# Performance work log

Measured on AMD Instinct MI355X. Metric: run time of the kernel, lower is better.

## Reference

```python
import jax, jax.numpy as jnp
import numpy as np

B, L, NS, D, M = 64, 200, 1000, 128, 50


def setup_inputs() -> dict:
    key = jax.random.key(0)
    ks = jax.random.split(key, 12)
    s = np.sqrt(2.0 / D).astype(np.float32)  # kaiming_normal scale for Mk/Mv0
    lw = np.sqrt(1.0 / D).astype(np.float32)
    return {
        "skills": jax.random.randint(ks[0], (B, L), 0, NS),
        "responses": jax.random.randint(ks[1], (B, L), 0, 2),
        "k_emb": jax.random.normal(ks[2], (NS, D), jnp.float32) * 0.02,
        "v_emb": jax.random.normal(ks[3], (2 * NS, D), jnp.float32) * 0.02,
        "Mk": jax.random.normal(ks[4], (M, D), jnp.float32) * s,
        "Mv0": jax.random.normal(ks[5], (M, D), jnp.float32) * s,
        "e_W": jax.random.normal(ks[6], (D, D), jnp.float32) * lw,
        "e_b": jnp.zeros((D,), jnp.float32),
        "a_W": jax.random.normal(ks[7], (D, D), jnp.float32) * lw,
        "a_b": jnp.zeros((D,), jnp.float32),
        "f_W": jax.random.normal(ks[8], (D, 2 * D), jnp.float32) * np.sqrt(1.0 / (2 * D)).astype(np.float32),
        "f_b": jnp.zeros((D,), jnp.float32),
        "p_W": jax.random.normal(ks[9], (1, D), jnp.float32) * lw,
        "p_b": jnp.zeros((1,), jnp.float32),
    }


def _dkvmn_forward(skills, responses, k_emb, v_emb, Mk, Mv0,
                   e_W, e_b, a_W, a_b, f_W, f_b, p_W, p_b):
    masked_r = responses * (responses > -1).astype(responses.dtype)
    x = skills + NS * masked_r                      # [B,L] combined (skill,response) id
    k = k_emb[skills]                               # [B,L,D]
    v = v_emb[x]                                    # [B,L,D]
    w = jax.nn.softmax(jnp.einsum('bld,md->blm', k, Mk), axis=-1)  # [B,L,M]
    e = jax.nn.sigmoid(v @ e_W.T + e_b)             # erase  [B,L,D]
    a = jnp.tanh(v @ a_W.T + a_b)                   # add    [B,L,D]

    def step(Mvt, wea):
        wt, et, at = wea                            # [B,M], [B,D], [B,D]
        u = wt[:, :, None]                          # [B,M,1]
        new = Mvt * (1.0 - u * et[:, None, :]) + u * at[:, None, :]
        return new, Mvt                             # emit PRE-update state (Mv[:, :-1])

    Mv_init = jnp.broadcast_to(Mv0[None], (B, M, D))
    _, Mv_pre = jax.lax.scan(
        step, Mv_init,
        (w.transpose(1, 0, 2), e.transpose(1, 0, 2), a.transpose(1, 0, 2)))
    # Mv_pre: [L,B,M,D]; weighted read of pre-update memory
    read = jnp.einsum('blm,lbmd->bld', w, Mv_pre)   # [B,L,D]
    f = jnp.tanh(jnp.concatenate([read, k], axis=-1) @ f_W.T + f_b)  # [B,L,D]
    p = jax.nn.sigmoid(f @ p_W.T + p_b)[..., 0]     # [B,L] (dropout off: eval)
    return p[:, 1:]                                 # pred, [B,L-1]


def reference(skills, responses, k_emb, v_emb, Mk, Mv0,
              e_W, e_b, a_W, a_b, f_W, f_b, p_W, p_b):
    return _dkvmn_forward(skills, responses, k_emb, v_emb, Mk, Mv0,
                          e_W, e_b, a_W, a_b, f_W, f_b, p_W, p_b)
```

## Files before the change

### kernel.cpp

```cpp
#include <hip/hip_runtime.h>
#include <hip/hip_bf16.h>

#define Bb 64
#define Ll 200
#define NSs 1000
#define Dd 128
#define Mm 50

__device__ __forceinline__ float bcast_lane(float v, int l) {
    return __int_as_float(__builtin_amdgcn_readlane(__float_as_int(v), l));
}

__global__ void __launch_bounds__(256) kern_wea(
        const int* __restrict__ skills,
        const int* __restrict__ responses,
        const float* __restrict__ k_emb,
        const float* __restrict__ v_emb,
        const float* __restrict__ Mk,
        const float* __restrict__ e_W, const float* __restrict__ e_b,
        const float* __restrict__ a_W, const float* __restrict__ a_b,
        float* __restrict__ w_out,
        float* __restrict__ e_out, float* __restrict__ a_out) {
    __shared__ float smem[12672];
    int tid = threadIdx.x;

    if (blockIdx.x >= 400) {
        int blk = blockIdx.x - 400;
        float (*mk)[Dd + 4] = (float(*)[Dd + 4])smem;
        float (*kr)[Dd + 4] = (float(*)[Dd + 4])(smem + 6600);

        for (int lin = tid; lin < (Mm * Dd) / 4; lin += 256) {
            float4 f = ((const float4*)Mk)[lin];
            *(float4*)&mk[lin >> 5][(lin & 31) * 4] = f;
        }
        for (int lin = tid; lin < 16 * 32; lin += 256) {
            int r  = lin >> 5;
            int c4 = lin & 31;
            int bl = blk * 16 + r;
            float4 f = ((const float4*)(k_emb + (size_t)skills[bl] * Dd))[c4];
            *(float4*)&kr[r][c4 * 4] = f;
        }
        __syncthreads();

        int wave = tid >> 6, lane = tid & 63;
        int mmr  = (lane < Mm) ? lane : 0;
        float acc[4] = {0.f, 0.f, 0.f, 0.f};
#pragma unroll 2
        for (int q = 0; q < 32; ++q) {
            float4 mkv = *(const float4*)&mk[mmr][q * 4];
#pragma unroll
            for (int i = 0; i < 4; ++i) {
                float4 kv = *(const float4*)&kr[wave * 4 + i][q * 4];
                acc[i] = fmaf(mkv.x, kv.x, acc[i]);
                acc[i] = fmaf(mkv.y, kv.y, acc[i]);
                acc[i] = fmaf(mkv.z, kv.z, acc[i]);
                acc[i] = fmaf(mkv.w, kv.w, acc[i]);
            }
        }
#pragma unroll
        for (int i = 0; i < 4; ++i) {
            float logit = (lane < Mm) ? acc[i] : -1e30f;
            float mx = logit;
            for (int off = 32; off > 0; off >>= 1) mx = fmaxf(mx, __shfl_down(mx, off));
            mx = __shfl(mx, 0);
            float ex = (lane < Mm) ? expf(logit - mx) : 0.f;
            float sm = ex;
            for (int off = 32; off > 0; off >>= 1) sm += __shfl_down(sm, off);
            sm = __shfl(sm, 0);
            int bl = blk * 16 + wave * 4 + i;
            if (lane < Mm) w_out[(size_t)bl * Mm + lane] = ex / sm;
        }
        return;
    }

    int blk = blockIdx.x;
    float (*vt)[Dd + 4] = (float(*)[Dd + 4])smem;
    float (*wt)[Dd + 4] = (float(*)[Dd + 4])(smem + 4224);

#pragma unroll
    for (int i = 0; i < 4; ++i) {
        int lin = i * 256 + tid;
        int r   = lin >> 5;
        int c4  = lin & 31;
        int bl  = blk * 32 + r;
        int rr  = responses[bl];
        int x   = skills[bl] + NSs * ((rr > -1) ? rr : 0);
        float4 f = ((const float4*)(v_emb + (size_t)x * Dd))[c4];
        *(float4*)&vt[r][c4 * 4] = f;
    }
    __syncthreads();

    int wave = tid >> 6, lane = tid & 63;
    int pg = lane >> 3, og = lane & 7;

    for (int s = 0; s < 4; ++s) {
        int base_row = wave * 64 + s * 16;
        bool is_e    = base_row < 128;
        const float* W = is_e ? e_W : a_W;
        int wrow0 = is_e ? base_row : base_row - 128;

#pragma unroll
        for (int i = 0; i < 8; ++i) {
            int lin = i * 64 + lane;
            int r   = lin >> 5;
            int c4  = lin & 31;
            float4 f = ((const float4*)(W + (size_t)(wrow0 + r) * Dd))[c4];
            *(float4*)&wt[wave * 16 + r][c4 * 4] = f;
        }

        float acc[4][2] = {};
#pragma unroll 2
        for (int q = 0; q < 32; ++q) {
            float4 av[4], bv[2];
#pragma unroll
            for (int i = 0; i < 4; ++i) av[i] = *(const float4*)&vt[pg + 8 * i][q * 4];
#pragma unroll
            for (int j = 0; j < 2; ++j) bv[j] = *(const float4*)&wt[wave * 16 + og + 8 * j][q * 4];
#pragma unroll
            for (int i = 0; i < 4; ++i)
#pragma unroll
                for (int j = 0; j < 2; ++j) {
                    acc[i][j] = fmaf(av[i].x, bv[j].x, acc[i][j]);
                    acc[i][j] = fmaf(av[i].y, bv[j].y, acc[i][j]);
                    acc[i][j] = fmaf(av[i].z, bv[j].z, acc[i][j]);
                    acc[i][j] = fmaf(av[i].w, bv[j].w, acc[i][j]);
                }
        }

        float* dst = is_e ? e_out : a_out;
#pragma unroll
        for (int j = 0; j < 2; ++j) {
            int row = wrow0 + og + 8 * j;
            float bias = (is_e ? e_b : a_b)[row];
#pragma unroll
            for (int i = 0; i < 4; ++i) {
                int bl = blk * 32 + pg + 8 * i;
                float v = acc[i][j] + bias;
                dst[(size_t)bl * Dd + row] = is_e ? (1.f / (1.f + expf(-v))) : tanhf(v);
            }
        }
    }
}

#define PQ_LOAD(S, tt) do { int _t = (tt);                                   \
    if (_t < T) { size_t _bl = blBase + _t;                                  \
        w##S = (lane < Mm) ? w_ws[_bl * Mm + lane] : 0.f;                    \
        e##S = e_ws[_bl * Dd + d];  a##S = a_ws[_bl * Dd + d]; } } while (0)

#define PQ_BODY(S) do {                                                      \
    _Pragma("unroll")                                                        \
    for (int m = 0; m < Mm; ++m) {                                           \
        float wm = bcast_lane(w##S, m);                                      \
        float A  = fmaf(-wm, e##S, 1.f);                                     \
        Q[m] = fmaf(A, Q[m], wm * a##S);                                     \
        P[m] *= A; } } while (0)

__global__ void __launch_bounds__(128) kern_scan_pq(
        const float* __restrict__ w_ws,
        const float* __restrict__ e_ws,
        const float* __restrict__ a_ws,
        float* __restrict__ P_ws, float* __restrict__ Q_ws,
        int C, int T) {
    int b = blockIdx.x / C, c = blockIdx.x % C;
    int d = threadIdx.x;
    int lane = d & 63;
    float P[Mm], Q[Mm];
#pragma unroll
    for (int m = 0; m < Mm; ++m) { P[m] = 1.f; Q[m] = 0.f; }

    size_t blBase = (size_t)b * Ll + (size_t)c * T;
    float w0 = 0.f, e0 = 0.f, a0 = 0.f;
    float w1 = 0.f, e1 = 0.f, a1 = 0.f;
    float w2 = 0.f, e2 = 0.f, a2 = 0.f;
    PQ_LOAD(0, 0);
    PQ_LOAD(1, 1);
    for (int tt = 0; tt < T; tt += 3) {
        PQ_LOAD(2, tt + 2);  PQ_BODY(0);
        if (tt + 1 < T) { PQ_LOAD(0, tt + 3);  PQ_BODY(1); }
        if (tt + 2 < T) { PQ_LOAD(1, tt + 4);  PQ_BODY(2); }
    }
    size_t base = ((size_t)(b * C + c)) * (Mm * Dd) + d;
#pragma unroll
    for (int m = 0; m < Mm; ++m) {
        P_ws[base + m * Dd] = P[m];
        Q_ws[base + m * Dd] = Q[m];
    }
}

template <int CC>
__global__ void kern_scan_comb_t(
        const float* __restrict__ Mv0,
        const float* __restrict__ P_ws, const float* __restrict__ Q_ws,
        float* __restrict__ S_ws) {
    int idx = blockIdx.x * 256 + threadIdx.x;
    int b   = idx / (Mm * Dd);
    int md  = idx % (Mm * Dd);
    float Pr[CC - 1], Qr[CC - 1];
#pragma unroll
    for (int c = 0; c < CC - 1; ++c) {
        size_t pq = ((size_t)(b * CC + c)) * (Mm * Dd) + md;
        Pr[c] = P_ws[pq];
        Qr[c] = Q_ws[pq];
    }
    float s = Mv0[md];
#pragma unroll
    for (int c = 0; c < CC - 1; ++c) {
        s = fmaf(Pr[c], s, Qr[c]);
        S_ws[((size_t)(b * (CC - 1) + c)) * (Mm * Dd) + md] = s;
    }
}

#define RD_BODY(S, tt) do {                                                  \
    float acc0 = 0.f, acc1 = 0.f;                                            \
    _Pragma("unroll")                                                        \
    for (int m = 0; m < Mm; m += 2) {                                        \
        float wm0 = bcast_lane(w##S, m);                                     \
        float wm1 = bcast_lane(w##S, m + 1);                                 \
        acc0 = fmaf(wm0, mv[m], acc0);                                       \
        mv[m] = fmaf(wm0, fmaf(-e##S, mv[m], a##S), mv[m]);                  \
        acc1 = fmaf(wm1, mv[m + 1], acc1);                                   \
        mv[m + 1] = fmaf(wm1, fmaf(-e##S, mv[m + 1], a##S), mv[m + 1]);      \
    }                                                                        \
    read_ws[(blBase + (tt)) * Dd + d] = acc0 + acc1;                         \
    } while (0)

__global__ void __launch_bounds__(128) kern_scan_rd(
        const float* __restrict__ Mv0,
        const float* __restrict__ S_ws,
        const float* __restrict__ w_ws,
        const float* __restrict__ e_ws,
        const float* __restrict__ a_ws,
        float* __restrict__ read_ws,
        int C, int T) {
    int b = blockIdx.x / C, c = blockIdx.x % C;
    int d = threadIdx.x;
    int lane = d & 63;
    float mv[Mm];
    if (c == 0) {
#pragma unroll
        for (int m = 0; m < Mm; ++m) mv[m] = Mv0[m * Dd + d];
    } else {
        size_t sb = ((size_t)(b * (C - 1) + (c - 1))) * (Mm * Dd) + d;
#pragma unroll
        for (int m = 0; m < Mm; ++m) mv[m] = S_ws[sb + m * Dd];
    }

    size_t blBase = (size_t)b * Ll + (size_t)c * T;
    float w0 = 0.f, e0 = 0.f, a0 = 0.f;
    float w1 = 0.f, e1 = 0.f, a1 = 0.f;
    float w2 = 0.f, e2 = 0.f, a2 = 0.f;
    PQ_LOAD(0, 0);
    PQ_LOAD(1, 1);
    for (int tt = 0; tt < T; tt += 3) {
        PQ_LOAD(2, tt + 2);  RD_BODY(0, tt);
        if (tt + 1 < T) { PQ_LOAD(0, tt + 3);  RD_BODY(1, tt + 1); }
        if (tt + 2 < T) { PQ_LOAD(1, tt + 4);  RD_BODY(2, tt + 2); }
    }
}

__global__ void __launch_bounds__(256) kern_out(
        const int* __restrict__ skills,
        const float* __restrict__ read_ws,
        const float* __restrict__ k_emb,
        const float* __restrict__ f_W, const float* __restrict__ f_b,
        const float* __restrict__ p_W, const float* __restrict__ p_b,
        float* __restrict__ out) {
    __shared__ float ct[32][2 * Dd + 4];
    __shared__ float wt[4][16][Dd + 4];
    __shared__ float pf[32][8];
    int tid = threadIdx.x;
    int blk = blockIdx.x;

#pragma unroll
    for (int i = 0; i < 8; ++i) {
        int lin = i * 256 + tid;
        int r   = lin >> 6;
        int c4  = lin & 63;
        int idx = blk * 32 + r;
        int b   = idx / (Ll - 1);
        int l   = idx % (Ll - 1) + 1;
        int bl  = b * Ll + l;
        float4 f;
        if (c4 < 32) f = ((const float4*)(read_ws + (size_t)bl * Dd))[c4];
        else         f = ((const float4*)(k_emb + (size_t)skills[bl] * Dd))[c4 - 32];
        *(float4*)&ct[r][c4 * 4] = f;
    }
    ((float*)pf)[tid] = 0.f;
    __syncthreads();

    int wave = tid >> 6, lane = tid & 63;
    int pg = lane >> 3, og = lane & 7;

    float ppart[4] = {0.f, 0.f, 0.f, 0.f};
    for (int sub = 0; sub < 2; ++sub) {
        float acc[4][2] = {};
        for (int h = 0; h < 2; ++h) {
#pragma unroll
            for (int i = 0; i < 8; ++i) {
                int lin = i * 64 + lane;
                int r   = lin >> 5;
                int c4  = lin & 31;
                float4 f = ((const float4*)(f_W +
                            (size_t)(wave * 32 + sub * 16 + r) * (2 * Dd)))[h * 32 + c4];
                *(float4*)&wt[wave][r][c4 * 4] = f;
            }
#pragma unroll 2
            for (int q = 0; q < 32; ++q) {
                int k = h * 128 + q * 4;
                float4 av[4], bv[2];
#pragma unroll
                for (int i = 0; i < 4; ++i) av[i] = *(const float4*)&ct[pg + 8 * i][k];
#pragma unroll
                for (int j = 0; j < 2; ++j) bv[j] = *(const float4*)&wt[wave][og + 8 * j][q * 4];
#pragma unroll
                for (int i = 0; i < 4; ++i)
#pragma unroll
                    for (int j = 0; j < 2; ++j) {
                        acc[i][j] = fmaf(av[i].x, bv[j].x, acc[i][j]);
                        acc[i][j] = fmaf(av[i].y, bv[j].y, acc[i][j]);
                        acc[i][j] = fmaf(av[i].z, bv[j].z, acc[i][j]);
                        acc[i][j] = fmaf(av[i].w, bv[j].w, acc[i][j]);
                    }
            }
        }
#pragma unroll
        for (int j = 0; j < 2; ++j) {
            int row = wave * 32 + sub * 16 + og + 8 * j;
            float fb = f_b[row];
            float pw = p_W[row];
#pragma unroll
            for (int i = 0; i < 4; ++i)
                ppart[i] = fmaf(tanhf(acc[i][j] + fb), pw, ppart[i]);
        }
    }
#pragma unroll
    for (int i = 0; i < 4; ++i) {
        float v = ppart[i];
        for (int off = 4; off > 0; off >>= 1) v += __shfl_down(v, off, 8);
        if (og == 0) pf[pg + 8 * i][wave] = v;
    }
    __syncthreads();
    if (tid < 32) {
        float s = pf[tid][0] + pf[tid][1] + pf[tid][2] + pf[tid][3] + p_b[0];
        out[blk * 32 + tid] = 1.f / (1.f + expf(-s));
    }
}

extern "C" void kernel_launch(void* const* d_in, const int* in_sizes, int n_in,
                              void* d_out, int out_size, void* d_ws, size_t ws_size,
                              hipStream_t stream) {
    const int*   skills    = (const int*)  d_in[0];
    const int*   responses = (const int*)  d_in[1];
    const float* k_emb     = (const float*)d_in[2];
    const float* v_emb     = (const float*)d_in[3];
    const float* Mk        = (const float*)d_in[4];
    const float* Mv0       = (const float*)d_in[5];
    const float* e_W       = (const float*)d_in[6];
    const float* e_b       = (const float*)d_in[7];
    const float* a_W       = (const float*)d_in[8];
    const float* a_b       = (const float*)d_in[9];
    const float* f_W       = (const float*)d_in[10];
    const float* f_b       = (const float*)d_in[11];
    const float* p_W       = (const float*)d_in[12];
    const float* p_b       = (const float*)d_in[13];
    (void)in_sizes; (void)n_in; (void)out_size;

    float* out = (float*)d_out;

    float* ws      = (float*)d_ws;
    float* w_ws    = ws;
    float* e_ws    = w_ws + (size_t)Bb * Ll * Mm;
    float* a_ws    = e_ws + (size_t)Bb * Ll * Dd;
    float* read_ws = a_ws + (size_t)Bb * Ll * Dd;
    float* extra   = read_ws + (size_t)Bb * Ll * Dd;

    const size_t baseF = (size_t)Bb * Ll * Mm + 3 * (size_t)Bb * Ll * Dd;
    const size_t BMD   = (size_t)Bb * Mm * Dd;
    int C = 1;
    const int cands[3] = {8, 5, 2};
    for (int i = 0; i < 3; ++i) {
        size_t need = (baseF + BMD * (3 * (size_t)cands[i] - 1)) * sizeof(float);
        if (ws_size >= need) { C = cands[i]; break; }
    }
    int T = Ll / C;
    float* P_ws = extra;
    float* Q_ws = P_ws + BMD * C;
    float* S_ws = Q_ws + BMD * C;

    kern_wea<<<400 + Bb * Ll / 16, 256, 0, stream>>>(skills, responses, k_emb, v_emb, Mk,
                                                     e_W, e_b, a_W, a_b, w_ws, e_ws, a_ws);
    if (C > 1) {
        kern_scan_pq<<<Bb * C, 128, 0, stream>>>(w_ws, e_ws, a_ws, P_ws, Q_ws, C, T);
        int cgrid = (int)(BMD / 256);
        if      (C == 8) kern_scan_comb_t<8><<<cgrid, 256, 0, stream>>>(Mv0, P_ws, Q_ws, S_ws);
        else if (C == 5) kern_scan_comb_t<5><<<cgrid, 256, 0, stream>>>(Mv0, P_ws, Q_ws, S_ws);
        else             kern_scan_comb_t<2><<<cgrid, 256, 0, stream>>>(Mv0, P_ws, Q_ws, S_ws);
    }
    kern_scan_rd<<<Bb * C, 128, 0, stream>>>(Mv0, S_ws, w_ws, e_ws, a_ws, read_ws, C, T);
    kern_out<<<Bb * (Ll - 1) / 32, 256, 0, stream>>>(skills, read_ws, k_emb,
                                                     f_W, f_b, p_W, p_b, out);
}
```

Before: 184.4 us.

## Fuse all five stages into one persistent kernel with grid barriers

Replaces the five separate launches (projection, chunked scan P/Q, combine, scan-read, output) with one persistent kernel of 256 blocks. The stages are separated by atomic grid-wide barriers and each stage loops over its work items. The aim is to remove launch gaps and tail effects between the small kernels. In exchange it adds barrier spin costs, fixes the chunk count at 8 without checking workspace size, and relies on all 256 blocks being resident at once.

```diff
diff --git a/kernel.cpp b/kernel.cpp
--- a/kernel.cpp
+++ b/kernel.cpp
@@ -6,140 +6,30 @@
 #define NSs 1000
 #define Dd 128
 #define Mm 50
+#define CC 8
+#define TT 25
+#define NBLK 256
 
 __device__ __forceinline__ float bcast_lane(float v, int l) {
     return __int_as_float(__builtin_amdgcn_readlane(__float_as_int(v), l));
 }
 
-__global__ void __launch_bounds__(256) kern_wea(
-        const int* __restrict__ skills,
-        const int* __restrict__ responses,
-        const float* __restrict__ k_emb,
-        const float* __restrict__ v_emb,
-        const float* __restrict__ Mk,
-        const float* __restrict__ e_W, const float* __restrict__ e_b,
-        const float* __restrict__ a_W, const float* __restrict__ a_b,
-        float* __restrict__ w_out,
-        float* __restrict__ e_out, float* __restrict__ a_out) {
-    __shared__ float smem[12672];
-    int tid = threadIdx.x;
-
-    if (blockIdx.x >= 400) {
-        int blk = blockIdx.x - 400;
-        float (*mk)[Dd + 4] = (float(*)[Dd + 4])smem;
-        float (*kr)[Dd + 4] = (float(*)[Dd + 4])(smem + 6600);
-
-        for (int lin = tid; lin < (Mm * Dd) / 4; lin += 256) {
-            float4 f = ((const float4*)Mk)[lin];
-            *(float4*)&mk[lin >> 5][(lin & 31) * 4] = f;
-        }
-        for (int lin = tid; lin < 16 * 32; lin += 256) {
-            int r  = lin >> 5;
-            int c4 = lin & 31;
-            int bl = blk * 16 + r;
-            float4 f = ((const float4*)(k_emb + (size_t)skills[bl] * Dd))[c4];
-            *(float4*)&kr[r][c4 * 4] = f;
-        }
-        __syncthreads();
-
-        int wave = tid >> 6, lane = tid & 63;
-        int mmr  = (lane < Mm) ? lane : 0;
-        float acc[4] = {0.f, 0.f, 0.f, 0.f};
-#pragma unroll 2
-        for (int q = 0; q < 32; ++q) {
-            float4 mkv = *(const float4*)&mk[mmr][q * 4];
-#pragma unroll
-            for (int i = 0; i < 4; ++i) {
-                float4 kv = *(const float4*)&kr[wave * 4 + i][q * 4];
-                acc[i] = fmaf(mkv.x, kv.x, acc[i]);
-                acc[i] = fmaf(mkv.y, kv.y, acc[i]);
-                acc[i] = fmaf(mkv.z, kv.z, acc[i]);
-                acc[i] = fmaf(mkv.w, kv.w, acc[i]);
-            }
-        }
-#pragma unroll
-        for (int i = 0; i < 4; ++i) {
-            float logit = (lane < Mm) ? acc[i] : -1e30f;
-            float mx = logit;
-            for (int off = 32; off > 0; off >>= 1) mx = fmaxf(mx, __shfl_down(mx, off));
-            mx = __shfl(mx, 0);
-            float ex = (lane < Mm) ? expf(logit - mx) : 0.f;
-            float sm = ex;
-            for (int off = 32; off > 0; off >>= 1) sm += __shfl_down(sm, off);
-            sm = __shfl(sm, 0);
-            int bl = blk * 16 + wave * 4 + i;
-            if (lane < Mm) w_out[(size_t)bl * Mm + lane] = ex / sm;
-        }
-        return;
-    }
-
-    int blk = blockIdx.x;
-    float (*vt)[Dd + 4] = (float(*)[Dd + 4])smem;
-    float (*wt)[Dd + 4] = (float(*)[Dd + 4])(smem + 4224);
-
-#pragma unroll
-    for (int i = 0; i < 4; ++i) {
-        int lin = i * 256 + tid;
-        int r   = lin >> 5;
-        int c4  = lin & 31;
-        int bl  = blk * 32 + r;
-        int rr  = responses[bl];
-        int x   = skills[bl] + NSs * ((rr > -1) ? rr : 0);
-        float4 f = ((const float4*)(v_emb + (size_t)x * Dd))[c4];
-        *(float4*)&vt[r][c4 * 4] = f;
-    }
+__device__ __forceinline__ void grid_barrier(int* bar, int nb) {
     __syncthreads();
-
-    int wave = tid >> 6, lane = tid & 63;
-    int pg = lane >> 3, og = lane & 7;
-
-    for (int s = 0; s < 4; ++s) {
-        int base_row = wave * 64 + s * 16;
-        bool is_e    = base_row < 128;
-        const float* W = is_e ? e_W : a_W;
-        int wrow0 = is_e ? base_row : base_row - 128;
-
-#pragma unroll
-        for (int i = 0; i < 8; ++i) {
-            int lin = i * 64 + lane;
-            int r   = lin >> 5;
-            int c4  = lin & 31;
-            float4 f = ((const float4*)(W + (size_t)(wrow0 + r) * Dd))[c4];
-            *(float4*)&wt[wave * 16 + r][c4 * 4] = f;
-        }
-
-        float acc[4][2] = {};
-#pragma unroll 2
-        for (int q = 0; q < 32; ++q) {
-            float4 av[4], bv[2];
-#pragma unroll
-            for (int i = 0; i < 4; ++i) av[i] = *(const float4*)&vt[pg + 8 * i][q * 4];
-#pragma unroll
-            for (int j = 0; j < 2; ++j) bv[j] = *(const float4*)&wt[wave * 16 + og + 8 * j][q * 4];
-#pragma unroll
-            for (int i = 0; i < 4; ++i)
-#pragma unroll
-                for (int j = 0; j < 2; ++j) {
-                    acc[i][j] = fmaf(av[i].x, bv[j].x, acc[i][j]);
-                    acc[i][j] = fmaf(av[i].y, bv[j].y, acc[i][j]);
-                    acc[i][j] = fmaf(av[i].z, bv[j].z, acc[i][j]);
-                    acc[i][j] = fmaf(av[i].w, bv[j].w, acc[i][j]);
-                }
-        }
-
-        float* dst = is_e ? e_out : a_out;
-#pragma unroll
-        for (int j = 0; j < 2; ++j) {
-            int row = wrow0 + og + 8 * j;
-            float bias = (is_e ? e_b : a_b)[row];
-#pragma unroll
-            for (int i = 0; i < 4; ++i) {
-                int bl = blk * 32 + pg + 8 * i;
-                float v = acc[i][j] + bias;
-                dst[(size_t)bl * Dd + row] = is_e ? (1.f / (1.f + expf(-v))) : tanhf(v);
-            }
-        }
-    }
+    __threadfence();
+    if (threadIdx.x == 0) {
+        int g = __hip_atomic_load(bar + 1, __ATOMIC_RELAXED, __HIP_MEMORY_SCOPE_AGENT);
+        int a = __hip_atomic_fetch_add(bar, 1, __ATOMIC_ACQ_REL, __HIP_MEMORY_SCOPE_AGENT);
+        if (a == nb - 1) {
+            __hip_atomic_store(bar, 0, __ATOMIC_RELAXED, __HIP_MEMORY_SCOPE_AGENT);
+            __hip_atomic_store(bar + 1, g + 1, __ATOMIC_RELEASE, __HIP_MEMORY_SCOPE_AGENT);
+        } else {
+            while (__hip_atomic_load(bar + 1, __ATOMIC_ACQUIRE, __HIP_MEMORY_SCOPE_AGENT) <= g)
+                __builtin_amdgcn_s_sleep(2);
+        }
+    }
+    __syncthreads();
+    __threadfence();
 }
 
 #define PQ_LOAD(S, tt) do { int _t = (tt);                                   \
@@ -154,61 +44,6 @@
         float A  = fmaf(-wm, e##S, 1.f);                                     \
         Q[m] = fmaf(A, Q[m], wm * a##S);                                     \
         P[m] *= A; } } while (0)
-
-__global__ void __launch_bounds__(128) kern_scan_pq(
-        const float* __restrict__ w_ws,
-        const float* __restrict__ e_ws,
-        const float* __restrict__ a_ws,
-        float* __restrict__ P_ws, float* __restrict__ Q_ws,
-        int C, int T) {
-    int b = blockIdx.x / C, c = blockIdx.x % C;
-    int d = threadIdx.x;
-    int lane = d & 63;
-    float P[Mm], Q[Mm];
-#pragma unroll
-    for (int m = 0; m < Mm; ++m) { P[m] = 1.f; Q[m] = 0.f; }
-
-    size_t blBase = (size_t)b * Ll + (size_t)c * T;
-    float w0 = 0.f, e0 = 0.f, a0 = 0.f;
-    float w1 = 0.f, e1 = 0.f, a1 = 0.f;
-    float w2 = 0.f, e2 = 0.f, a2 = 0.f;
-    PQ_LOAD(0, 0);
-    PQ_LOAD(1, 1);
-    for (int tt = 0; tt < T; tt += 3) {
-        PQ_LOAD(2, tt + 2);  PQ_BODY(0);
-        if (tt + 1 < T) { PQ_LOAD(0, tt + 3);  PQ_BODY(1); }
-        if (tt + 2 < T) { PQ_LOAD(1, tt + 4);  PQ_BODY(2); }
-    }
-    size_t base = ((size_t)(b * C + c)) * (Mm * Dd) + d;
-#pragma unroll
-    for (int m = 0; m < Mm; ++m) {
-        P_ws[base + m * Dd] = P[m];
-        Q_ws[base + m * Dd] = Q[m];
-    }
-}
-
-template <int CC>
-__global__ void kern_scan_comb_t(
-        const float* __restrict__ Mv0,
-        const float* __restrict__ P_ws, const float* __restrict__ Q_ws,
-        float* __restrict__ S_ws) {
-    int idx = blockIdx.x * 256 + threadIdx.x;
-    int b   = idx / (Mm * Dd);
-    int md  = idx % (Mm * Dd);
-    float Pr[CC - 1], Qr[CC - 1];
-#pragma unroll
-    for (int c = 0; c < CC - 1; ++c) {
-        size_t pq = ((size_t)(b * CC + c)) * (Mm * Dd) + md;
-        Pr[c] = P_ws[pq];
-        Qr[c] = Q_ws[pq];
-    }
-    float s = Mv0[md];
-#pragma unroll
-    for (int c = 0; c < CC - 1; ++c) {
-        s = fmaf(Pr[c], s, Qr[c]);
-        S_ws[((size_t)(b * (CC - 1) + c)) * (Mm * Dd) + md] = s;
-    }
-}
 
 #define RD_BODY(S, tt) do {                                                  \
     float acc0 = 0.f, acc1 = 0.f;                                            \
@@ -224,125 +59,282 @@
     read_ws[(blBase + (tt)) * Dd + d] = acc0 + acc1;                         \
     } while (0)
 
-__global__ void __launch_bounds__(128) kern_scan_rd(
+__global__ void __launch_bounds__(256, 2) kern_mega(
+        const int* __restrict__ skills,
+        const int* __restrict__ responses,
+        const float* __restrict__ k_emb,
+        const float* __restrict__ v_emb,
+        const float* __restrict__ Mk,
         const float* __restrict__ Mv0,
-        const float* __restrict__ S_ws,
-        const float* __restrict__ w_ws,
-        const float* __restrict__ e_ws,
-        const float* __restrict__ a_ws,
-        float* __restrict__ read_ws,
-        int C, int T) {
-    int b = blockIdx.x / C, c = blockIdx.x % C;
-    int d = threadIdx.x;
-    int lane = d & 63;
-    float mv[Mm];
-    if (c == 0) {
-#pragma unroll
-        for (int m = 0; m < Mm; ++m) mv[m] = Mv0[m * Dd + d];
-    } else {
-        size_t sb = ((size_t)(b * (C - 1) + (c - 1))) * (Mm * Dd) + d;
-#pragma unroll
-        for (int m = 0; m < Mm; ++m) mv[m] = S_ws[sb + m * Dd];
-    }
-
-    size_t blBase = (size_t)b * Ll + (size_t)c * T;
-    float w0 = 0.f, e0 = 0.f, a0 = 0.f;
-    float w1 = 0.f, e1 = 0.f, a1 = 0.f;
-    float w2 = 0.f, e2 = 0.f, a2 = 0.f;
-    PQ_LOAD(0, 0);
-    PQ_LOAD(1, 1);
-    for (int tt = 0; tt < T; tt += 3) {
-        PQ_LOAD(2, tt + 2);  RD_BODY(0, tt);
-        if (tt + 1 < T) { PQ_LOAD(0, tt + 3);  RD_BODY(1, tt + 1); }
-        if (tt + 2 < T) { PQ_LOAD(1, tt + 4);  RD_BODY(2, tt + 2); }
-    }
-}
-
-__global__ void __launch_bounds__(256) kern_out(
-        const int* __restrict__ skills,
-        const float* __restrict__ read_ws,
-        const float* __restrict__ k_emb,
+        const float* __restrict__ e_W, const float* __restrict__ e_b,
+        const float* __restrict__ a_W, const float* __restrict__ a_b,
         const float* __restrict__ f_W, const float* __restrict__ f_b,
         const float* __restrict__ p_W, const float* __restrict__ p_b,
-        float* __restrict__ out) {
-    __shared__ float ct[32][2 * Dd + 4];
-    __shared__ float wt[4][16][Dd + 4];
-    __shared__ float pf[32][8];
-    int tid = threadIdx.x;
-    int blk = blockIdx.x;
-
-#pragma unroll
-    for (int i = 0; i < 8; ++i) {
-        int lin = i * 256 + tid;
-        int r   = lin >> 6;
-        int c4  = lin & 63;
-        int idx = blk * 32 + r;
-        int b   = idx / (Ll - 1);
-        int l   = idx % (Ll - 1) + 1;
-        int bl  = b * Ll + l;
-        float4 f;
-        if (c4 < 32) f = ((const float4*)(read_ws + (size_t)bl * Dd))[c4];
-        else         f = ((const float4*)(k_emb + (size_t)skills[bl] * Dd))[c4 - 32];
-        *(float4*)&ct[r][c4 * 4] = f;
-    }
-    ((float*)pf)[tid] = 0.f;
-    __syncthreads();
-
-    int wave = tid >> 6, lane = tid & 63;
-    int pg = lane >> 3, og = lane & 7;
-
-    float ppart[4] = {0.f, 0.f, 0.f, 0.f};
-    for (int sub = 0; sub < 2; ++sub) {
-        float acc[4][2] = {};
-        for (int h = 0; h < 2; ++h) {
-#pragma unroll
-            for (int i = 0; i < 8; ++i) {
-                int lin = i * 64 + lane;
-                int r   = lin >> 5;
-                int c4  = lin & 31;
-                float4 f = ((const float4*)(f_W +
-                            (size_t)(wave * 32 + sub * 16 + r) * (2 * Dd)))[h * 32 + c4];
-                *(float4*)&wt[wave][r][c4 * 4] = f;
-            }
+        float* __restrict__ w_ws, float* __restrict__ e_ws, float* __restrict__ a_ws,
+        float* __restrict__ read_ws,
+        float* __restrict__ P_ws, float* __restrict__ Q_ws, float* __restrict__ S_ws,
+        float* __restrict__ out, int* bar) {
+    __shared__ float smem[17024];
+    int tid  = threadIdx.x;
+    int blk  = blockIdx.x;
+    int wave = tid >> 6, lane64 = tid & 63;
+
+    for (int v = blk; v < 1200; v += NBLK) {
+        if (v >= 400) {
+            int wblk = v - 400;
+            float (*mk)[Dd + 4] = (float(*)[Dd + 4])smem;
+            float (*kr)[Dd + 4] = (float(*)[Dd + 4])(smem + 6600);
+            for (int lin = tid; lin < (Mm * Dd) / 4; lin += 256) {
+                float4 f = ((const float4*)Mk)[lin];
+                *(float4*)&mk[lin >> 5][(lin & 31) * 4] = f;
+            }
+            for (int lin = tid; lin < 16 * 32; lin += 256) {
+                int r = lin >> 5, c4 = lin & 31;
+                int bl = wblk * 16 + r;
+                float4 f = ((const float4*)(k_emb + (size_t)skills[bl] * Dd))[c4];
+                *(float4*)&kr[r][c4 * 4] = f;
+            }
+            __syncthreads();
+            int mmr = (lane64 < Mm) ? lane64 : 0;
+            float acc[4] = {0.f, 0.f, 0.f, 0.f};
 #pragma unroll 2
             for (int q = 0; q < 32; ++q) {
-                int k = h * 128 + q * 4;
-                float4 av[4], bv[2];
-#pragma unroll
-                for (int i = 0; i < 4; ++i) av[i] = *(const float4*)&ct[pg + 8 * i][k];
-#pragma unroll
-                for (int j = 0; j < 2; ++j) bv[j] = *(const float4*)&wt[wave][og + 8 * j][q * 4];
+                float4 mkv = *(const float4*)&mk[mmr][q * 4];
+#pragma unroll
+                for (int i = 0; i < 4; ++i) {
+                    float4 kv = *(const float4*)&kr[wave * 4 + i][q * 4];
+                    acc[i] = fmaf(mkv.x, kv.x, acc[i]);
+                    acc[i] = fmaf(mkv.y, kv.y, acc[i]);
+                    acc[i] = fmaf(mkv.z, kv.z, acc[i]);
+                    acc[i] = fmaf(mkv.w, kv.w, acc[i]);
+                }
+            }
+#pragma unroll
+            for (int i = 0; i < 4; ++i) {
+                float logit = (lane64 < Mm) ? acc[i] : -1e30f;
+                float mx = logit;
+                for (int off = 32; off > 0; off >>= 1) mx = fmaxf(mx, __shfl_down(mx, off));
+                mx = __shfl(mx, 0);
+                float ex = (lane64 < Mm) ? expf(logit - mx) : 0.f;
+                float sm = ex;
+                for (int off = 32; off > 0; off >>= 1) sm += __shfl_down(sm, off);
+                sm = __shfl(sm, 0);
+                int bl = wblk * 16 + wave * 4 + i;
+                if (lane64 < Mm) w_ws[(size_t)bl * Mm + lane64] = ex / sm;
+            }
+        } else {
+            float (*vt)[Dd + 4] = (float(*)[Dd + 4])smem;
+            float (*wt)[Dd + 4] = (float(*)[Dd + 4])(smem + 4224);
+#pragma unroll
+            for (int i = 0; i < 4; ++i) {
+                int lin = i * 256 + tid;
+                int r = lin >> 5, c4 = lin & 31;
+                int bl = v * 32 + r;
+                int rr = responses[bl];
+                int x  = skills[bl] + NSs * ((rr > -1) ? rr : 0);
+                float4 f = ((const float4*)(v_emb + (size_t)x * Dd))[c4];
+                *(float4*)&vt[r][c4 * 4] = f;
+            }
+            __syncthreads();
+            int pg = lane64 >> 3, og = lane64 & 7;
+            for (int s = 0; s < 4; ++s) {
+                int base_row = wave * 64 + s * 16;
+                bool is_e = base_row < 128;
+                const float* W = is_e ? e_W : a_W;
+                int wrow0 = is_e ? base_row : base_row - 128;
+#pragma unroll
+                for (int i = 0; i < 8; ++i) {
+                    int lin = i * 64 + lane64;
+                    int r = lin >> 5, c4 = lin & 31;
+                    float4 f = ((const float4*)(W + (size_t)(wrow0 + r) * Dd))[c4];
+                    *(float4*)&wt[wave * 16 + r][c4 * 4] = f;
+                }
+                float acc[4][2] = {};
+#pragma unroll 2
+                for (int q = 0; q < 32; ++q) {
+                    float4 av[4], bv[2];
+#pragma unroll
+                    for (int i = 0; i < 4; ++i) av[i] = *(const float4*)&vt[pg + 8 * i][q * 4];
+#pragma unroll
+                    for (int j = 0; j < 2; ++j) bv[j] = *(const float4*)&wt[wave * 16 + og + 8 * j][q * 4];
+#pragma unroll
+                    for (int i = 0; i < 4; ++i)
+#pragma unroll
+                        for (int j = 0; j < 2; ++j) {
+                            acc[i][j] = fmaf(av[i].x, bv[j].x, acc[i][j]);
+                            acc[i][j] = fmaf(av[i].y, bv[j].y, acc[i][j]);
+                            acc[i][j] = fmaf(av[i].z, bv[j].z, acc[i][j]);
+                            acc[i][j] = fmaf(av[i].w, bv[j].w, acc[i][j]);
+                        }
+                }
+                float* dst = is_e ? e_ws : a_ws;
+#pragma unroll
+                for (int j = 0; j < 2; ++j) {
+                    int row = wrow0 + og + 8 * j;
+                    float bias = (is_e ? e_b : a_b)[row];
+#pragma unroll
+                    for (int i = 0; i < 4; ++i) {
+                        int bl = v * 32 + pg + 8 * i;
+                        float val = acc[i][j] + bias;
+                        dst[(size_t)bl * Dd + row] = is_e ? (1.f / (1.f + expf(-val))) : tanhf(val);
+                    }
+                }
+            }
+        }
+        __syncthreads();
+    }
+
+    grid_barrier(bar, NBLK);
+
+    {
+        int hs = tid >> 7;
+        int d  = tid & 127;
+        int lane = d & 63;
+        int h = blk * 2 + hs;
+        int b = h >> 3, c = h & 7;
+        const int T = TT;
+        float P[Mm], Q[Mm];
+#pragma unroll
+        for (int m = 0; m < Mm; ++m) { P[m] = 1.f; Q[m] = 0.f; }
+        size_t blBase = (size_t)b * Ll + (size_t)c * T;
+        float w0 = 0.f, e0 = 0.f, a0 = 0.f;
+        float w1 = 0.f, e1 = 0.f, a1 = 0.f;
+        float w2 = 0.f, e2 = 0.f, a2 = 0.f;
+        PQ_LOAD(0, 0);
+        PQ_LOAD(1, 1);
+        for (int tt = 0; tt < T; tt += 3) {
+            PQ_LOAD(2, tt + 2);  PQ_BODY(0);
+            if (tt + 1 < T) { PQ_LOAD(0, tt + 3);  PQ_BODY(1); }
+            if (tt + 2 < T) { PQ_LOAD(1, tt + 4);  PQ_BODY(2); }
+        }
+        size_t base = ((size_t)(b * CC + c)) * (Mm * Dd) + d;
+#pragma unroll
+        for (int m = 0; m < Mm; ++m) {
+            P_ws[base + m * Dd] = P[m];
+            Q_ws[base + m * Dd] = Q[m];
+        }
+    }
+
+    grid_barrier(bar, NBLK);
+
+    for (int idx = blk * 256 + tid; idx < Bb * Mm * Dd; idx += NBLK * 256) {
+        int b  = idx / (Mm * Dd);
+        int md = idx % (Mm * Dd);
+        float s = Mv0[md];
+        for (int c = 0; c < CC - 1; ++c) {
+            size_t pq = ((size_t)(b * CC + c)) * (Mm * Dd) + md;
+            s = fmaf(P_ws[pq], s, Q_ws[pq]);
+            S_ws[((size_t)(b * (CC - 1) + c)) * (Mm * Dd) + md] = s;
+        }
+    }
+
+    grid_barrier(bar, NBLK);
+
+    {
+        int hs = tid >> 7;
+        int d  = tid & 127;
+        int lane = d & 63;
+        int h = blk * 2 + hs;
+        int b = h >> 3, c = h & 7;
+        const int T = TT;
+        float mv[Mm];
+        if (c == 0) {
+#pragma unroll
+            for (int m = 0; m < Mm; ++m) mv[m] = Mv0[m * Dd + d];
+        } else {
+            size_t sb = ((size_t)(b * (CC - 1) + (c - 1))) * (Mm * Dd) + d;
+#pragma unroll
+            for (int m = 0; m < Mm; ++m) mv[m] = S_ws[sb + m * Dd];
+        }
+        size_t blBase = (size_t)b * Ll + (size_t)c * T;
+        float w0 = 0.f, e0 = 0.f, a0 = 0.f;
+        float w1 = 0.f, e1 = 0.f, a1 = 0.f;
+        float w2 = 0.f, e2 = 0.f, a2 = 0.f;
+        PQ_LOAD(0, 0);
+        PQ_LOAD(1, 1);
+        for (int tt = 0; tt < T; tt += 3) {
+            PQ_LOAD(2, tt + 2);  RD_BODY(0, tt);
+            if (tt + 1 < T) { PQ_LOAD(0, tt + 3);  RD_BODY(1, tt + 1); }
+            if (tt + 2 < T) { PQ_LOAD(1, tt + 4);  RD_BODY(2, tt + 2); }
+        }
+    }
+
+    grid_barrier(bar, NBLK);
+
+    for (int v = blk; v < 398; v += NBLK) {
+        float (*ct)[2 * Dd + 4] = (float(*)[2 * Dd + 4])smem;
+        float (*wt)[Dd + 4]     = (float(*)[Dd + 4])(smem + 8320);
+        float (*pf)[8]          = (float(*)[8])(smem + 16768);
+#pragma unroll
+        for (int i = 0; i < 8; ++i) {
+            int lin = i * 256 + tid;
+            int r = lin >> 6, c4 = lin & 63;
+            int idx = v * 32 + r;
+            int b = idx / (Ll - 1);
+            int l = idx % (Ll - 1) + 1;
+            int bl = b * Ll + l;
+            float4 f;
+            if (c4 < 32) f = ((const float4*)(read_ws + (size_t)bl * Dd))[c4];
+            else         f = ((const float4*)(k_emb + (size_t)skills[bl] * Dd))[c4 - 32];
+            *(float4*)&ct[r][c4 * 4] = f;
+        }
+        ((float*)pf)[tid] = 0.f;
+        __syncthreads();
+
+        int pg = lane64 >> 3, og = lane64 & 7;
+        float ppart[4] = {0.f, 0.f, 0.f, 0.f};
+        for (int sub = 0; sub < 2; ++sub) {
+            float acc[4][2] = {};
+            for (int hh = 0; hh < 2; ++hh) {
+#pragma unroll
+                for (int i = 0; i < 8; ++i) {
+                    int lin = i * 64 + lane64;
+                    int r = lin >> 5, c4 = lin & 31;
+                    float4 f = ((const float4*)(f_W +
+                                (size_t)(wave * 32 + sub * 16 + r) * (2 * Dd)))[hh * 32 + c4];
+                    *(float4*)&wt[wave * 16 + r][c4 * 4] = f;
+                }
+#pragma unroll 2
+                for (int q = 0; q < 32; ++q) {
+                    int k = hh * 128 + q * 4;
+                    float4 av[4], bv[2];
+#pragma unroll
+                    for (int i = 0; i < 4; ++i) av[i] = *(const float4*)&ct[pg + 8 * i][k];
+#pragma unroll
+                    for (int j = 0; j < 2; ++j) bv[j] = *(const float4*)&wt[wave * 16 + og + 8 * j][q * 4];
+#pragma unroll
+                    for (int i = 0; i < 4; ++i)
+#pragma unroll
+                        for (int j = 0; j < 2; ++j) {
+                            acc[i][j] = fmaf(av[i].x, bv[j].x, acc[i][j]);
+                            acc[i][j] = fmaf(av[i].y, bv[j].y, acc[i][j]);
+                            acc[i][j] = fmaf(av[i].z, bv[j].z, acc[i][j]);
+                            acc[i][j] = fmaf(av[i].w, bv[j].w, acc[i][j]);
+                        }
+                }
+            }
+#pragma unroll
+            for (int j = 0; j < 2; ++j) {
+                int row = wave * 32 + sub * 16 + og + 8 * j;
+                float fb = f_b[row];
+                float pw = p_W[row];
 #pragma unroll
                 for (int i = 0; i < 4; ++i)
-#pragma unroll
-                    for (int j = 0; j < 2; ++j) {
-                        acc[i][j] = fmaf(av[i].x, bv[j].x, acc[i][j]);
-                        acc[i][j] = fmaf(av[i].y, bv[j].y, acc[i][j]);
-                        acc[i][j] = fmaf(av[i].z, bv[j].z, acc[i][j]);
-                        acc[i][j] = fmaf(av[i].w, bv[j].w, acc[i][j]);
-                    }
-            }
-        }
-#pragma unroll
-        for (int j = 0; j < 2; ++j) {
-            int row = wave * 32 + sub * 16 + og + 8 * j;
-            float fb = f_b[row];
-            float pw = p_W[row];
-#pragma unroll
-            for (int i = 0; i < 4; ++i)
-                ppart[i] = fmaf(tanhf(acc[i][j] + fb), pw, ppart[i]);
-        }
-    }
-#pragma unroll
-    for (int i = 0; i < 4; ++i) {
-        float v = ppart[i];
-        for (int off = 4; off > 0; off >>= 1) v += __shfl_down(v, off, 8);
-        if (og == 0) pf[pg + 8 * i][wave] = v;
-    }
-    __syncthreads();
-    if (tid < 32) {
-        float s = pf[tid][0] + pf[tid][1] + pf[tid][2] + pf[tid][3] + p_b[0];
-        out[blk * 32 + tid] = 1.f / (1.f + expf(-s));
+                    ppart[i] = fmaf(tanhf(acc[i][j] + fb), pw, ppart[i]);
+            }
+        }
+#pragma unroll
+        for (int i = 0; i < 4; ++i) {
+            float val = ppart[i];
+            for (int off = 4; off > 0; off >>= 1) val += __shfl_down(val, off, 8);
+            if (og == 0) pf[pg + 8 * i][wave] = val;
+        }
+        __syncthreads();
+        if (tid < 32) {
+            float s = pf[tid][0] + pf[tid][1] + pf[tid][2] + pf[tid][3] + p_b[0];
+            out[v * 32 + tid] = 1.f / (1.f + expf(-s));
+        }
+        __syncthreads();
     }
 }
 
@@ -363,40 +355,27 @@
     const float* f_b       = (const float*)d_in[11];
     const float* p_W       = (const float*)d_in[12];
     const float* p_b       = (const float*)d_in[13];
-    (void)in_sizes; (void)n_in; (void)out_size;
+    (void)in_sizes; (void)n_in; (void)out_size; (void)ws_size;
 
     float* out = (float*)d_out;
+
+    const size_t BLM = (size_t)Bb * Ll * Mm;
+    const size_t BLD = (size_t)Bb * Ll * Dd;
+    const size_t BMD = (size_t)Bb * Mm * Dd;
 
     float* ws      = (float*)d_ws;
     float* w_ws    = ws;
-    float* e_ws    = w_ws + (size_t)Bb * Ll * Mm;
-    float* a_ws    = e_ws + (size_t)Bb * Ll * Dd;
-    float* read_ws = a_ws + (size_t)Bb * Ll * Dd;
-    float* extra   = read_ws + (size_t)Bb * Ll * Dd;
-
-    const size_t baseF = (size_t)Bb * Ll * Mm + 3 * (size_t)Bb * Ll * Dd;
-    const size_t BMD   = (size_t)Bb * Mm * Dd;
-    int C = 1;
-    const int cands[3] = {8, 5, 2};
-    for (int i = 0; i < 3; ++i) {
-        size_t need = (baseF + BMD * (3 * (size_t)cands[i] - 1)) * sizeof(float);
-        if (ws_size >= need) { C = cands[i]; break; }
-    }
-    int T = Ll / C;
-    float* P_ws = extra;
-    float* Q_ws = P_ws + BMD * C;
-    float* S_ws = Q_ws + BMD * C;
-
-    kern_wea<<<400 + Bb * Ll / 16, 256, 0, stream>>>(skills, responses, k_emb, v_emb, Mk,
-                                                     e_W, e_b, a_W, a_b, w_ws, e_ws, a_ws);
-    if (C > 1) {
-        kern_scan_pq<<<Bb * C, 128, 0, stream>>>(w_ws, e_ws, a_ws, P_ws, Q_ws, C, T);
-        int cgrid = (int)(BMD / 256);
-        if      (C == 8) kern_scan_comb_t<8><<<cgrid, 256, 0, stream>>>(Mv0, P_ws, Q_ws, S_ws);
-        else if (C == 5) kern_scan_comb_t<5><<<cgrid, 256, 0, stream>>>(Mv0, P_ws, Q_ws, S_ws);
-        else             kern_scan_comb_t<2><<<cgrid, 256, 0, stream>>>(Mv0, P_ws, Q_ws, S_ws);
-    }
-    kern_scan_rd<<<Bb * C, 128, 0, stream>>>(Mv0, S_ws, w_ws, e_ws, a_ws, read_ws, C, T);
-    kern_out<<<Bb * (Ll - 1) / 32, 256, 0, stream>>>(skills, read_ws, k_emb,
-                                                     f_W, f_b, p_W, p_b, out);
+    float* e_ws    = w_ws + BLM;
+    float* a_ws    = e_ws + BLD;
+    float* read_ws = a_ws + BLD;
+    float* P_ws    = read_ws + BLD;
+    float* Q_ws    = P_ws + BMD * CC;
+    float* S_ws    = Q_ws + BMD * CC;
+    int*   bar     = (int*)(S_ws + BMD * (CC - 1));
+
+    hipMemsetAsync(bar, 0, 2 * sizeof(int), stream);
+    kern_mega<<<NBLK, 256, 0, stream>>>(skills, responses, k_emb, v_emb, Mk, Mv0,
+                                        e_W, e_b, a_W, a_b, f_W, f_b, p_W, p_b,
+                                        w_ws, e_ws, a_ws, read_ws, P_ws, Q_ws, S_ws,
+                                        out, bar);
 }
```

Result: slower. 482.8 us (+161.9%).
